# Optimization experiments

Measured on AMD Instinct MI355X. Metric: run time of the kernel, lower is better.

Reference implementation:

```python
import jax, jax.numpy as jnp
import numpy as np

N_NODES = 100000
N_EDGES = 1600000
IN_DIM, HID_DIM, OUT_DIM, N_CLASSES = 128, 256, 256, 200
N_GRAPHS = 64


def gcn_conv(x, edge_index, W, b):
    """PyG GCNConv: add self-loops, symmetric deg^{-1/2} normalization,
    aggregate source->target, then bias. Linear transform applied first
    (cheaper since in/out dims comparable)."""
    N = x.shape[0]
    loop = jnp.arange(N, dtype=edge_index.dtype)
    src = jnp.concatenate([edge_index[0], loop])
    dst = jnp.concatenate([edge_index[1], loop])
    deg = jax.ops.segment_sum(jnp.ones_like(dst, dtype=x.dtype), dst, num_segments=N)
    dinv = jnp.where(deg > 0, jax.lax.rsqrt(deg), 0.0)
    xw = x @ W  # [N, F_out]
    norm = dinv[src] * dinv[dst]  # [E+N]
    msg = xw[src] * norm[:, None]  # gather + scale
    out = jax.ops.segment_sum(msg, dst, num_segments=N)  # scatter-add
    return out + b


def global_mean_pool(x, batch, num_graphs):
    sums = jax.ops.segment_sum(x, batch, num_segments=num_graphs)
    cnt = jax.ops.segment_sum(jnp.ones((x.shape[0],), x.dtype), batch, num_segments=num_graphs)
    return sums / jnp.maximum(cnt, 1.0)[:, None]


def setup_inputs() -> dict:
    key = jax.random.key(0)
    ks = jax.random.split(key, 8)
    x = jax.random.normal(ks[0], (N_NODES, IN_DIM), dtype=jnp.float32)
    edge_index = jax.random.randint(ks[1], (2, N_EDGES), 0, N_NODES, dtype=jnp.int32)
    batch = jnp.sort(jax.random.randint(ks[2], (N_NODES,), 0, N_GRAPHS, dtype=jnp.int32))
    # Glorot-style init for weights (scaled normals)
    W1 = jax.random.normal(ks[3], (IN_DIM, HID_DIM), dtype=jnp.float32) / np.sqrt(IN_DIM)
    b1 = jnp.zeros((HID_DIM,), jnp.float32)
    W2 = jax.random.normal(ks[4], (HID_DIM, OUT_DIM), dtype=jnp.float32) / np.sqrt(HID_DIM)
    b2 = jnp.zeros((OUT_DIM,), jnp.float32)
    Wc = jax.random.normal(ks[5], (OUT_DIM, N_CLASSES), dtype=jnp.float32) / np.sqrt(OUT_DIM)
    bc = jnp.zeros((N_CLASSES,), jnp.float32)
    return {"x": x, "edge_index": edge_index, "batch": batch, "num_graphs": N_GRAPHS,
            "W1": W1, "b1": b1, "W2": W2, "b2": b2, "Wc": Wc, "bc": bc}


def reference(x, edge_index, batch, num_graphs, W1, b1, W2, b2, Wc, bc):
    h = jax.nn.relu(gcn_conv(x, edge_index, W1, b1))
    # dropout p=0.5 is identity in eval mode
    h = jax.nn.relu(gcn_conv(h, edge_index, W2, b2))
    g = global_mean_pool(h, batch, num_graphs)  # [num_graphs, OUT_DIM]
    return g @ Wc + bc  # [num_graphs, N_CLASSES]
```

## Files before the change

kernel.cpp:

```cpp
#include <hip/hip_runtime.h>
#include <cstdint>
#include <cstddef>


typedef __attribute__((ext_vector_type(8))) short bf16x8;
typedef __attribute__((ext_vector_type(4))) float f32x4;

#define P1_CHUNK 4096
#define BCAP 8192

__device__ inline unsigned short f2bf(float f) {
    unsigned u = __float_as_uint(f);
    u = (u + 0x7FFFu + ((u >> 16) & 1u)) >> 16;
    return (unsigned short)u;
}
__device__ inline unsigned nib4(unsigned u) {
    return (u & 15u) | (((u >> 8) & 15u) << 4) | (((u >> 16) & 15u) << 8) |
           (((u >> 24) & 15u) << 12);
}
__device__ inline unsigned nibexp(unsigned h) {
    unsigned t = (h | (h << 8)) & 0x00FF00FFu;
    return (t | (t << 4)) & 0x0F0F0F0Fu;
}
__device__ inline float ub(unsigned u, int q) { return (float)((u >> (8 * q)) & 255u); }

__global__ __launch_bounds__(256) void scatter_prep_kernel(
        const int* __restrict__ src, const int* __restrict__ dst,
        int* __restrict__ bucketCnt, unsigned* __restrict__ pairs, int E, int NB, int EB,
        const float* __restrict__ W1, unsigned short* __restrict__ WT1, int K1,
        const float* __restrict__ W2, unsigned short* __restrict__ WT2,
        const int* __restrict__ batch, int* __restrict__ cnt, int N, int HB,
        const float* __restrict__ x, unsigned char* __restrict__ Y0q,
        float* __restrict__ scaleRaw) {
    __shared__ int hist[512];
    __shared__ int base[512];
    int bid = blockIdx.x, t = threadIdx.x;
    if (bid < EB) {
        int e0 = bid * P1_CHUNK;
        int eend = min(e0 + P1_CHUNK, E);
        for (int i = t; i < NB; i += 256) hist[i] = 0;
        __syncthreads();
        for (int e = e0 + t; e < eend; e += 256) atomicAdd(&hist[dst[e] >> 8], 1);
        __syncthreads();
        for (int i = t; i < NB; i += 256) {
            int c = hist[i];
            base[i] = (c > 0) ? atomicAdd(&bucketCnt[i], c) : 0;
            hist[i] = 0;
        }
        __syncthreads();
        for (int e = e0 + t; e < eend; e += 256) {
            int d = dst[e], s = src[e];
            int b = d >> 8;
            int r = base[b] + atomicAdd(&hist[b], 1);
            if (r < BCAP)
                pairs[(size_t)b * BCAP + r] = (unsigned)s | ((unsigned)(d & 255) << 24);
        }
    } else if (bid < EB + K1) {
        int idx = (bid - EB) * 256 + t;
        int k = idx >> 8, n = idx & 255;
        WT1[n * K1 + k] = f2bf(W1[idx]);
    } else if (bid < EB + K1 + 256) {
        int idx = (bid - EB - K1) * 256 + t;
        int k = idx >> 8, n = idx & 255;
        WT2[n * 256 + k] = f2bf(W2[idx]);
    } else if (bid < EB + K1 + 256 + HB) {
        hist[t] = 0;
        __syncthreads();
        int n = (bid - EB - K1 - 256) * 256 + t;
        if (n < N) atomicAdd(&hist[batch[n]], 1);
        __syncthreads();
        if (hist[t] != 0) atomicAdd(&cnt[t], hist[t]);
    } else {
        int node = (bid - EB - K1 - 256 - HB) * 4 + (t >> 6);
        int lane = t & 63;
        if (node < N) {
            float2 v = reinterpret_cast<const float2*>(x)[(size_t)node * 64 + lane];
            float m = fmaxf(fabsf(v.x), fabsf(v.y));
            #pragma unroll
            for (int d = 32; d >= 1; d >>= 1) m = fmaxf(m, __shfl_xor(m, d, 64));
            float qinv = m > 0.f ? 7.f / m : 0.f;
            int q0 = min(max((int)rintf(v.x * qinv) + 8, 0), 15);
            int q1 = min(max((int)rintf(v.y * qinv) + 8, 0), 15);
            Y0q[(size_t)node * 64 + lane] = (unsigned char)(q0 | (q1 << 4));
            if (lane == 0) scaleRaw[node] = m * (1.f / 7.f);
        }
    }
}

__global__ __launch_bounds__(256) void fine_place_kernel(
        const unsigned* __restrict__ pairs, const int* __restrict__ bucketCnt,
        int* __restrict__ off, float* __restrict__ dinv,
        const float* __restrict__ scaleRaw, float* __restrict__ scale0,
        int* __restrict__ csr, int N, int E) {
    __shared__ int hist[256];
    __shared__ int loff[256];
    __shared__ int ws[4];
    __shared__ int sbase;
    int b = blockIdx.x, t = threadIdx.x;
    int lane = t & 63, w = t >> 6;

    int part = 0;
    for (int i = t; i < b; i += 256) part += bucketCnt[i];
    #pragma unroll
    for (int d = 1; d < 64; d <<= 1) part += __shfl_xor(part, d, 64);
    if (lane == 0) ws[w] = part;
    __syncthreads();
    if (t == 0) sbase = ws[0] + ws[1] + ws[2] + ws[3];
    if (b == 0 && t == 0) off[N] = E;
    __syncthreads();
    int base = sbase;

    int cnt = min(bucketCnt[b], BCAP);
    const unsigned* pp = pairs + (size_t)b * BCAP;
    hist[t] = 0;
    __syncthreads();
    for (int i = t; i < cnt; i += 256) atomicAdd(&hist[pp[i] >> 24], 1);
    __syncthreads();
    int v = hist[t];
    {
        int x = v;
        #pragma unroll
        for (int d = 1; d < 64; d <<= 1) {
            int y = __shfl_up(x, d, 64);
            if (lane >= d) x += y;
        }
        if (lane == 63) ws[w] = x;
        __syncthreads();
        int woff = 0;
        #pragma unroll
        for (int j = 0; j < 4; j++)
            if (j < w) woff += ws[j];
        loff[t] = woff + x - v;
    }
    int node = b * 256 + t;
    if (node < N) {
        off[node] = base + loff[t];
        float di = rsqrtf((float)v + 1.0f);
        dinv[node] = di;
        scale0[node] = di * scaleRaw[node];
    }
    __syncthreads();
    hist[t] = 0;
    __syncthreads();
    for (int i = t; i < cnt; i += 256) {
        unsigned pr = pp[i];
        int dl = pr >> 24;
        int r = atomicAdd(&hist[dl], 1);
        csr[base + loff[dl] + r] = (int)(pr & 0xFFFFFFu);
    }
}

__global__ __launch_bounds__(256) void aggregate_q4x_kernel(
        const unsigned char* __restrict__ Q, const float* __restrict__ scale,
        unsigned short* __restrict__ OUT,
        const int* __restrict__ off, const int* __restrict__ csr,
        const float* __restrict__ dinv, int N) {
    int node = __builtin_amdgcn_readfirstlane(blockIdx.x * 4 + (threadIdx.x >> 6));
    int lane = threadIdx.x & 63;
    if (node >= N) return;

    float acc0, acc1, ssum;
    auto loadpay = [&](int s) -> unsigned {
        return (unsigned)Q[(size_t)s * 64 + lane];
    };
    auto lo = [&](unsigned b) -> float { return (float)(b & 15u); };
    auto hi = [&](unsigned b) -> float { return (float)((b >> 4) & 15u); };
    {
        unsigned v = loadpay(node);
        float sc = scale[node];
        acc0 = sc * lo(v);
        acc1 = sc * hi(v);
        ssum = sc;
    }
    int e0 = off[node], e1 = off[node + 1];
    int e = e0;
    for (; e + 16 <= e1; e += 16) {
        int s[16]; unsigned v[16]; float sc[16];
        #pragma unroll
        for (int j = 0; j < 16; j++) s[j] = csr[e + j];
        #pragma unroll
        for (int j = 0; j < 16; j++) { v[j] = loadpay(s[j]); sc[j] = scale[s[j]]; }
        #pragma unroll
        for (int j = 0; j < 16; j++) {
            ssum += sc[j];
            acc0 += sc[j] * lo(v[j]);
            acc1 += sc[j] * hi(v[j]);
        }
    }
    if (e + 8 <= e1) {
        int s[8]; unsigned v[8]; float sc[8];
        #pragma unroll
        for (int j = 0; j < 8; j++) s[j] = csr[e + j];
        #pragma unroll
        for (int j = 0; j < 8; j++) { v[j] = loadpay(s[j]); sc[j] = scale[s[j]]; }
        #pragma unroll
        for (int j = 0; j < 8; j++) {
            ssum += sc[j];
            acc0 += sc[j] * lo(v[j]);
            acc1 += sc[j] * hi(v[j]);
        }
        e += 8;
    }
    for (; e < e1; e++) {
        int s = csr[e];
        unsigned v = loadpay(s);
        float sc = scale[s];
        ssum += sc;
        acc0 += sc * lo(v);
        acc1 += sc * hi(v);
    }
    float corr = 8.f * ssum;
    float di = dinv[node];
    unsigned o = (unsigned)f2bf(di * (acc0 - corr)) |
                 ((unsigned)f2bf(di * (acc1 - corr)) << 16);
    reinterpret_cast<unsigned*>(OUT)[(size_t)node * 64 + lane] = o;
}

__global__ __launch_bounds__(256) void aggregate_q4_kernel(
        const unsigned short* __restrict__ Q4, const float* __restrict__ scale,
        unsigned short* __restrict__ OUT,
        const int* __restrict__ off, const int* __restrict__ csr,
        const float* __restrict__ dinv, int N) {
    int node = __builtin_amdgcn_readfirstlane(blockIdx.x * 4 + (threadIdx.x >> 6));
    int lane = threadIdx.x & 63;
    if (node >= N) return;

    float acc[4];
    auto loadpay = [&](int s) -> unsigned {
        return (unsigned)Q4[(size_t)s * 64 + lane];
    };
    {
        unsigned u = nibexp(loadpay(node));
        float sc = scale[node];
        #pragma unroll
        for (int q = 0; q < 4; q++) acc[q] = sc * ub(u, q);
    }
    int e0 = off[node], e1 = off[node + 1];
    int e = e0;
    for (; e + 16 <= e1; e += 16) {
        int s[16]; unsigned v[16]; float sc[16];
        #pragma unroll
        for (int j = 0; j < 16; j++) s[j] = csr[e + j];
        #pragma unroll
        for (int j = 0; j < 16; j++) { v[j] = loadpay(s[j]); sc[j] = scale[s[j]]; }
        #pragma unroll
        for (int j = 0; j < 16; j++) {
            unsigned u = nibexp(v[j]);
            #pragma unroll
            for (int q = 0; q < 4; q++) acc[q] += sc[j] * ub(u, q);
        }
    }
    if (e + 8 <= e1) {
        int s[8]; unsigned v[8]; float sc[8];
        #pragma unroll
        for (int j = 0; j < 8; j++) s[j] = csr[e + j];
        #pragma unroll
        for (int j = 0; j < 8; j++) { v[j] = loadpay(s[j]); sc[j] = scale[s[j]]; }
        #pragma unroll
        for (int j = 0; j < 8; j++) {
            unsigned u = nibexp(v[j]);
            #pragma unroll
            for (int q = 0; q < 4; q++) acc[q] += sc[j] * ub(u, q);
        }
        e += 8;
    }
    for (; e < e1; e++) {
        int s = csr[e];
        unsigned u = nibexp(loadpay(s));
        float sc = scale[s];
        #pragma unroll
        for (int q = 0; q < 4; q++) acc[q] += sc * ub(u, q);
    }
    float di = dinv[node];
    uint2 o;
    o.x = (unsigned)f2bf(di * acc[0]) | ((unsigned)f2bf(di * acc[1]) << 16);
    o.y = (unsigned)f2bf(di * acc[2]) | ((unsigned)f2bf(di * acc[3]) << 16);
    reinterpret_cast<uint2*>(OUT)[(size_t)node * 64 + lane] = o;
}

template <int K, int MODE>
__global__ __launch_bounds__(256) void mfma_gemm_kernel(
        const unsigned short* __restrict__ A, const unsigned short* __restrict__ WT,
        const float* __restrict__ bias, const float* __restrict__ dinv,
        char* __restrict__ Cq, float* __restrict__ scaleOut,
        const int* __restrict__ batch, float* __restrict__ gsum, int M) {
    constexpr int KK = K / 32;
    constexpr int RB = K * 2;
    constexpr int CHUNKS = 64 * RB / 16;
    constexpr int EXTRA = (MODE == 0) ? (256 * 4 + 64 * 4 + 64 * 256) : 16;
    __shared__ __align__(16) char As[64 * RB];
    __shared__ __align__(16) char extra[EXTRA];

    const int t = threadIdx.x;
    const int lane = t & 63, w = t >> 6;
    const int lhi = lane >> 4, l15 = lane & 15;
    const int r0 = blockIdx.x * 64;

    bf16x8 breg[4][KK];
    #pragma unroll
    for (int nf = 0; nf < 4; nf++)
        #pragma unroll
        for (int kk = 0; kk < KK; kk++)
            breg[nf][kk] = *reinterpret_cast<const bf16x8*>(
                WT + (size_t)(w * 64 + nf * 16 + l15) * K + kk * 32 + lhi * 8);
    float bn[4];
    #pragma unroll
    for (int nf = 0; nf < 4; nf++) bn[nf] = bias[w * 64 + nf * 16 + l15];

    #pragma unroll
    for (int p = 0; p < CHUNKS / 256; p++) {
        int idx = p * 256 + t;
        int row = idx / (RB / 16);
        int cb = idx % (RB / 16);
        int sbyte = (cb * 16) ^ ((row & 7) << 4);
        const char* g = (const char*)(A + (size_t)(r0 + row) * K) + sbyte;
        __builtin_amdgcn_global_load_lds(
            (const __attribute__((address_space(1))) void*)g,
            (__attribute__((address_space(3))) void*)(As + idx * 16),
            16, 0, 0);
    }
    __syncthreads();

    f32x4 acc[4][4];
    #pragma unroll
    for (int i = 0; i < 4; i++)
        #pragma unroll
        for (int j = 0; j < 4; j++) acc[i][j] = (f32x4){0.f, 0.f, 0.f, 0.f};

    #pragma unroll
    for (int kk = 0; kk < KK; kk++) {
        bf16x8 a[4];
        int kb = (kk * 32 + lhi * 8) * 2;
        #pragma unroll
        for (int mf = 0; mf < 4; mf++) {
            int row = mf * 16 + l15;
            a[mf] = *reinterpret_cast<const bf16x8*>(
                As + row * RB + (kb ^ ((row & 7) << 4)));
        }
        #pragma unroll
        for (int mf = 0; mf < 4; mf++)
            #pragma unroll
            for (int nf = 0; nf < 4; nf++)
                acc[mf][nf] = __builtin_amdgcn_mfma_f32_16x16x32_bf16(
                    a[mf], breg[nf][kk], acc[mf][nf], 0, 0, 0);
    }

    if constexpr (MODE == 0) {
        float* wmax = (float*)extra;
        float* qinv = wmax + 256;
        char* pack = (char*)(qinv + 64);
        #pragma unroll
        for (int mf = 0; mf < 4; mf++)
            #pragma unroll
            for (int j = 0; j < 4; j++) {
                float lmax = 0.f;
                #pragma unroll
                for (int nf = 0; nf < 4; nf++) {
                    float v = fmaxf(acc[mf][nf][j] + bn[nf], 0.f);
                    acc[mf][nf][j] = v;
                    lmax = fmaxf(lmax, v);
                }
                lmax = fmaxf(lmax, __shfl_xor(lmax, 1, 64));
                lmax = fmaxf(lmax, __shfl_xor(lmax, 2, 64));
                lmax = fmaxf(lmax, __shfl_xor(lmax, 4, 64));
                lmax = fmaxf(lmax, __shfl_xor(lmax, 8, 64));
                if (l15 == 0) wmax[w * 64 + mf * 16 + lhi * 4 + j] = lmax;
            }
        __syncthreads();
        if (t < 64) {
            float m4 = fmaxf(fmaxf(wmax[t], wmax[64 + t]),
                             fmaxf(wmax[128 + t], wmax[192 + t]));
            qinv[t] = m4 > 0.f ? 15.f / m4 : 0.f;
            if (r0 + t < M) scaleOut[r0 + t] = dinv[r0 + t] * m4 * (1.f / 15.f);
        }
        __syncthreads();
        #pragma unroll
        for (int mf = 0; mf < 4; mf++)
            #pragma unroll
            for (int j = 0; j < 4; j++) {
                int r = mf * 16 + lhi * 4 + j;
                float qi = qinv[r];
                #pragma unroll
                for (int nf = 0; nf < 4; nf++)
                    pack[r * 256 + w * 64 + nf * 16 + l15] =
                        (char)min((int)rintf(acc[mf][nf][j] * qi), 15);
            }
        __syncthreads();
        #pragma unroll
        for (int p = 0; p < 4; p++) {
            int idx = p * 256 + t;
            uint4 s4 = reinterpret_cast<const uint4*>(pack)[idx];
            uint2 o;
            o.x = nib4(s4.x) | (nib4(s4.y) << 16);
            o.y = nib4(s4.z) | (nib4(s4.w) << 16);
            reinterpret_cast<uint2*>(Cq + (size_t)r0 * 128)[idx] = o;
        }
    } else {
        int gmin = batch[min(r0, M - 1)];
        int gmax = batch[min(r0 + 63, M - 1)];
        if (gmin == gmax) {
            #pragma unroll
            for (int nf = 0; nf < 4; nf++) {
                float s = 0.f;
                #pragma unroll
                for (int mf = 0; mf < 4; mf++)
                    #pragma unroll
                    for (int j = 0; j < 4; j++) {
                        int m = r0 + mf * 16 + lhi * 4 + j;
                        float v = fmaxf(acc[mf][nf][j] + bn[nf], 0.f);
                        s += (m < M) ? v : 0.f;
                    }
                s += __shfl_xor(s, 16, 64);
                s += __shfl_xor(s, 32, 64);
                if (lhi == 0)
                    atomicAdd(&gsum[(size_t)gmin * 256 + w * 64 + nf * 16 + l15], s);
            }
        } else {
            #pragma unroll
            for (int mf = 0; mf < 4; mf++)
                #pragma unroll
                for (int j = 0; j < 4; j++) {
                    int m = r0 + mf * 16 + lhi * 4 + j;
                    if (m < M) {
                        int g = batch[m];
                        #pragma unroll
                        for (int nf = 0; nf < 4; nf++)
                            atomicAdd(&gsum[(size_t)g * 256 + w * 64 + nf * 16 + l15],
                                      fmaxf(acc[mf][nf][j] + bn[nf], 0.f));
                    }
                }
        }
    }
}

__global__ __launch_bounds__(256) void pool_final_kernel(const float* __restrict__ gsum,
                                                         const int* __restrict__ cnt,
                                                         const float* __restrict__ Wc,
                                                         const float* __restrict__ bc,
                                                         float* __restrict__ out) {
    __shared__ float gm[256];
    int g = blockIdx.x, t = threadIdx.x;
    float inv = 1.0f / fmaxf((float)cnt[g], 1.0f);
    gm[t] = gsum[g * 256 + t] * inv;
    __syncthreads();
    if (t < 200) {
        float acc = bc[t];
        #pragma unroll 8
        for (int k = 0; k < 256; k++) acc += gm[k] * Wc[k * 200 + t];
        out[g * 200 + t] = acc;
    }
}

extern "C" void kernel_launch(void* const* d_in, const int* in_sizes, int n_in,
                              void* d_out, int out_size, void* d_ws, size_t ws_size,
                              hipStream_t stream) {
    const float* x   = (const float*)d_in[0];
    const int* ei    = (const int*)d_in[1];
    const int* batch = (const int*)d_in[2];
    const float* W1  = (const float*)d_in[4];
    const float* b1  = (const float*)d_in[5];
    const float* W2  = (const float*)d_in[6];
    const float* b2  = (const float*)d_in[7];
    const float* Wc  = (const float*)d_in[8];
    const float* bc  = (const float*)d_in[9];
    float* out = (float*)d_out;

    const int N = in_sizes[2];
    const int E = in_sizes[1] / 2;
    const int G = out_size / 200;
    const int K1 = in_sizes[0] / N;
    const int Mpad = (N + 63) & ~63;
    const int NB = (N + 255) >> 8;
    const int ntiles = Mpad / 64;
    const int EB = (E + P1_CHUNK - 1) / P1_CHUNK;
    const int* src = ei;
    const int* dst = ei + E;

    char* p = (char*)d_ws;
    auto alloc = [&](size_t bytes) -> char* {
        char* r = p;
        p += (bytes + 255) & ~(size_t)255;
        return r;
    };
    int*   off      = (int*)alloc((size_t)(N + 1) * 4);
    int*   bktCnt   = (int*)alloc((size_t)NB * 4);
    int*   cnt      = (int*)alloc(256 * 4);
    float* dinv     = (float*)alloc((size_t)N * 4);
    float* scaleRaw = (float*)alloc((size_t)N * 4);
    float* scale0   = (float*)alloc((size_t)N * 4);
    float* scale1   = (float*)alloc((size_t)N * 4);
    float* gsum     = (float*)alloc((size_t)G * 256 * 4);
    int*   csr      = (int*)alloc((size_t)E * 4);
    unsigned* pairs = (unsigned*)alloc((size_t)NB * BCAP * 4);
    unsigned short* WT1 = (unsigned short*)alloc((size_t)256 * K1 * 2);
    unsigned short* WT2 = (unsigned short*)alloc((size_t)256 * 256 * 2);
    unsigned char*  Y0q4 = (unsigned char*)alloc((size_t)N * 64);
    char*           Y1q4 = alloc((size_t)Mpad * 128);
    unsigned short* a1   = (unsigned short*)alloc((size_t)Mpad * K1 * 2);
    unsigned short* a2   = (unsigned short*)alloc((size_t)Mpad * 256 * 2);

    hipMemsetAsync(bktCnt, 0, (size_t)NB * 4, stream);
    hipMemsetAsync(cnt, 0, 256 * 4, stream);
    hipMemsetAsync(gsum, 0, (size_t)G * 256 * 4, stream);

    int blkN = (N + 255) / 256;
    int PB = (N + 3) / 4;
    scatter_prep_kernel<<<EB + K1 + 256 + blkN + PB, 256, 0, stream>>>(
        src, dst, bktCnt, pairs, E, NB, EB, W1, WT1, K1, W2, WT2,
        batch, cnt, N, blkN, x, Y0q4, scaleRaw);
    fine_place_kernel<<<NB, 256, 0, stream>>>(
        pairs, bktCnt, off, dinv, scaleRaw, scale0, csr, N, E);

    aggregate_q4x_kernel<<<(N + 3) / 4, 256, 0, stream>>>(
        Y0q4, scale0, a1, off, csr, dinv, N);
    mfma_gemm_kernel<128, 0><<<ntiles, 256, 0, stream>>>(
        a1, WT1, b1, dinv, Y1q4, scale1, nullptr, nullptr, N);
    aggregate_q4_kernel<<<(N + 3) / 4, 256, 0, stream>>>(
        (const unsigned short*)Y1q4, scale1, a2, off, csr, dinv, N);
    mfma_gemm_kernel<256, 1><<<ntiles, 256, 0, stream>>>(
        a2, WT2, b2, nullptr, nullptr, nullptr, batch, gsum, N);
    pool_final_kernel<<<G, 256, 0, stream>>>(gsum, cnt, Wc, bc, out);
}
```

Baseline: 269.9 us.

## Overlap GEMM tiles with aggregation chunks via fused role-split kernels

Splits each layer's node range into three chunks and launches fused kernels in which one block in seventeen runs a GEMM tile for the previous chunk while the remaining blocks aggregate the next chunk. The goal is to hide the compute-bound MFMA GEMM behind the memory-bound gather. Fused GEMM blocks load weights from global memory per MFMA instead of holding them in registers, which keeps the fused kernel's register use within the occupancy hint but re-reads weights inside the inner loop. The change also adds more launches and a large shared-memory footprint to the aggregation blocks, which may lower their occupancy.

```diff
diff --git a/kernel.cpp b/kernel.cpp
--- a/kernel.cpp
+++ b/kernel.cpp
@@ -150,27 +150,20 @@
     }
 }
 
-__global__ __launch_bounds__(256) void aggregate_q4x_kernel(
+
+__device__ __forceinline__ void agg_q4x_body(
         const unsigned char* __restrict__ Q, const float* __restrict__ scale,
         unsigned short* __restrict__ OUT,
         const int* __restrict__ off, const int* __restrict__ csr,
-        const float* __restrict__ dinv, int N) {
-    int node = __builtin_amdgcn_readfirstlane(blockIdx.x * 4 + (threadIdx.x >> 6));
-    int lane = threadIdx.x & 63;
-    if (node >= N) return;
-
+        const float* __restrict__ dinv, int node, int lane) {
     float acc0, acc1, ssum;
-    auto loadpay = [&](int s) -> unsigned {
-        return (unsigned)Q[(size_t)s * 64 + lane];
-    };
+    auto loadpay = [&](int s) -> unsigned { return (unsigned)Q[(size_t)s * 64 + lane]; };
     auto lo = [&](unsigned b) -> float { return (float)(b & 15u); };
     auto hi = [&](unsigned b) -> float { return (float)((b >> 4) & 15u); };
     {
         unsigned v = loadpay(node);
         float sc = scale[node];
-        acc0 = sc * lo(v);
-        acc1 = sc * hi(v);
-        ssum = sc;
+        acc0 = sc * lo(v); acc1 = sc * hi(v); ssum = sc;
     }
     int e0 = off[node], e1 = off[node + 1];
     int e = e0;
@@ -181,11 +174,7 @@
         #pragma unroll
         for (int j = 0; j < 16; j++) { v[j] = loadpay(s[j]); sc[j] = scale[s[j]]; }
         #pragma unroll
-        for (int j = 0; j < 16; j++) {
-            ssum += sc[j];
-            acc0 += sc[j] * lo(v[j]);
-            acc1 += sc[j] * hi(v[j]);
-        }
+        for (int j = 0; j < 16; j++) { ssum += sc[j]; acc0 += sc[j] * lo(v[j]); acc1 += sc[j] * hi(v[j]); }
     }
     if (e + 8 <= e1) {
         int s[8]; unsigned v[8]; float sc[8];
@@ -194,20 +183,14 @@
         #pragma unroll
         for (int j = 0; j < 8; j++) { v[j] = loadpay(s[j]); sc[j] = scale[s[j]]; }
         #pragma unroll
-        for (int j = 0; j < 8; j++) {
-            ssum += sc[j];
-            acc0 += sc[j] * lo(v[j]);
-            acc1 += sc[j] * hi(v[j]);
-        }
+        for (int j = 0; j < 8; j++) { ssum += sc[j]; acc0 += sc[j] * lo(v[j]); acc1 += sc[j] * hi(v[j]); }
         e += 8;
     }
     for (; e < e1; e++) {
         int s = csr[e];
         unsigned v = loadpay(s);
         float sc = scale[s];
-        ssum += sc;
-        acc0 += sc * lo(v);
-        acc1 += sc * hi(v);
+        ssum += sc; acc0 += sc * lo(v); acc1 += sc * hi(v);
     }
     float corr = 8.f * ssum;
     float di = dinv[node];
@@ -216,19 +199,13 @@
     reinterpret_cast<unsigned*>(OUT)[(size_t)node * 64 + lane] = o;
 }
 
-__global__ __launch_bounds__(256) void aggregate_q4_kernel(
+__device__ __forceinline__ void agg_q4_body(
         const unsigned short* __restrict__ Q4, const float* __restrict__ scale,
         unsigned short* __restrict__ OUT,
         const int* __restrict__ off, const int* __restrict__ csr,
-        const float* __restrict__ dinv, int N) {
-    int node = __builtin_amdgcn_readfirstlane(blockIdx.x * 4 + (threadIdx.x >> 6));
-    int lane = threadIdx.x & 63;
-    if (node >= N) return;
-
+        const float* __restrict__ dinv, int node, int lane) {
     float acc[4];
-    auto loadpay = [&](int s) -> unsigned {
-        return (unsigned)Q4[(size_t)s * 64 + lane];
-    };
+    auto loadpay = [&](int s) -> unsigned { return (unsigned)Q4[(size_t)s * 64 + lane]; };
     {
         unsigned u = nibexp(loadpay(node));
         float sc = scale[node];
@@ -278,31 +255,31 @@
     reinterpret_cast<uint2*>(OUT)[(size_t)node * 64 + lane] = o;
 }
 
-template <int K, int MODE>
-__global__ __launch_bounds__(256) void mfma_gemm_kernel(
+template <int K, int MODE, bool BREG>
+__device__ __forceinline__ void gemm_body(
         const unsigned short* __restrict__ A, const unsigned short* __restrict__ WT,
         const float* __restrict__ bias, const float* __restrict__ dinv,
         char* __restrict__ Cq, float* __restrict__ scaleOut,
-        const int* __restrict__ batch, float* __restrict__ gsum, int M) {
+        const int* __restrict__ batch, float* __restrict__ gsum,
+        int M, int r0, char* As, char* extra) {
     constexpr int KK = K / 32;
     constexpr int RB = K * 2;
     constexpr int CHUNKS = 64 * RB / 16;
-    constexpr int EXTRA = (MODE == 0) ? (256 * 4 + 64 * 4 + 64 * 256) : 16;
-    __shared__ __align__(16) char As[64 * RB];
-    __shared__ __align__(16) char extra[EXTRA];
-
     const int t = threadIdx.x;
     const int lane = t & 63, w = t >> 6;
     const int lhi = lane >> 4, l15 = lane & 15;
-    const int r0 = blockIdx.x * 64;
-
+
+    auto bload = [&](int nf, int kk) -> bf16x8 {
+        return *reinterpret_cast<const bf16x8*>(
+            WT + (size_t)(w * 64 + nf * 16 + l15) * K + kk * 32 + lhi * 8);
+    };
     bf16x8 breg[4][KK];
-    #pragma unroll
-    for (int nf = 0; nf < 4; nf++)
-        #pragma unroll
-        for (int kk = 0; kk < KK; kk++)
-            breg[nf][kk] = *reinterpret_cast<const bf16x8*>(
-                WT + (size_t)(w * 64 + nf * 16 + l15) * K + kk * 32 + lhi * 8);
+    if constexpr (BREG) {
+        #pragma unroll
+        for (int nf = 0; nf < 4; nf++)
+            #pragma unroll
+            for (int kk = 0; kk < KK; kk++) breg[nf][kk] = bload(nf, kk);
+    }
     float bn[4];
     #pragma unroll
     for (int nf = 0; nf < 4; nf++) bn[nf] = bias[w * 64 + nf * 16 + l15];
@@ -340,9 +317,13 @@
         #pragma unroll
         for (int mf = 0; mf < 4; mf++)
             #pragma unroll
-            for (int nf = 0; nf < 4; nf++)
+            for (int nf = 0; nf < 4; nf++) {
+                bf16x8 bv;
+                if constexpr (BREG) bv = breg[nf][kk];
+                else bv = bload(nf, kk);
                 acc[mf][nf] = __builtin_amdgcn_mfma_f32_16x16x32_bf16(
-                    a[mf], breg[nf][kk], acc[mf][nf], 0, 0, 0);
+                    a[mf], bv, acc[mf][nf], 0, 0, 0);
+            }
     }
 
     if constexpr (MODE == 0) {
@@ -430,6 +411,87 @@
                     }
                 }
         }
+    }
+}
+
+
+__global__ __launch_bounds__(256) void aggregate_q4x_kernel(
+        const unsigned char* __restrict__ Q, const float* __restrict__ scale,
+        unsigned short* __restrict__ OUT,
+        const int* __restrict__ off, const int* __restrict__ csr,
+        const float* __restrict__ dinv, int nodeStart, int nodeEnd) {
+    int node = __builtin_amdgcn_readfirstlane(nodeStart + blockIdx.x * 4 + (threadIdx.x >> 6));
+    if (node < nodeEnd)
+        agg_q4x_body(Q, scale, OUT, off, csr, dinv, node, threadIdx.x & 63);
+}
+
+__global__ __launch_bounds__(256) void aggregate_q4_kernel(
+        const unsigned short* __restrict__ Q4, const float* __restrict__ scale,
+        unsigned short* __restrict__ OUT,
+        const int* __restrict__ off, const int* __restrict__ csr,
+        const float* __restrict__ dinv, int nodeStart, int nodeEnd) {
+    int node = __builtin_amdgcn_readfirstlane(nodeStart + blockIdx.x * 4 + (threadIdx.x >> 6));
+    if (node < nodeEnd)
+        agg_q4_body(Q4, scale, OUT, off, csr, dinv, node, threadIdx.x & 63);
+}
+
+template <int K, int MODE>
+__global__ __launch_bounds__(256) void mfma_gemm_kernel(
+        const unsigned short* __restrict__ A, const unsigned short* __restrict__ WT,
+        const float* __restrict__ bias, const float* __restrict__ dinv,
+        char* __restrict__ Cq, float* __restrict__ scaleOut,
+        const int* __restrict__ batch, float* __restrict__ gsum, int M, int rowStart) {
+    __shared__ __align__(16) char As[64 * K * 2];
+    __shared__ __align__(16) char extra[(MODE == 0) ? (256 * 4 + 64 * 4 + 64 * 256) : 16];
+    gemm_body<K, MODE, true>(A, WT, bias, dinv, Cq, scaleOut, batch, gsum,
+                             M, rowStart + blockIdx.x * 64, As, extra);
+}
+
+__device__ __forceinline__ bool role_split(int bid, int G, int& gemmIdx, int& aggIdx) {
+    if (bid % 17 == 0 && bid / 17 < G) { gemmIdx = bid / 17; return true; }
+    aggIdx = bid - min((bid + 16) / 17, G);
+    return false;
+}
+
+__global__ __launch_bounds__(256, 4) void fused_l1_kernel(
+        const unsigned char* __restrict__ Q0, const float* __restrict__ scale0,
+        unsigned short* __restrict__ a1,
+        const int* __restrict__ off, const int* __restrict__ csr,
+        const float* __restrict__ dinv,
+        const unsigned short* __restrict__ WT1, const float* __restrict__ b1,
+        char* __restrict__ Y1q4, float* __restrict__ scale1,
+        int N, int gemmTiles, int aggStart, int aggEnd, int gemmStart) {
+    __shared__ __align__(16) char As[64 * 256];
+    __shared__ __align__(16) char extra[256 * 4 + 64 * 4 + 64 * 256];
+    int gi, ai;
+    if (role_split(blockIdx.x, gemmTiles, gi, ai)) {
+        gemm_body<128, 0, false>(a1, WT1, b1, dinv, Y1q4, scale1, nullptr, nullptr,
+                                 N, gemmStart + gi * 64, As, extra);
+    } else {
+        int node = __builtin_amdgcn_readfirstlane(aggStart + ai * 4 + (threadIdx.x >> 6));
+        if (node < aggEnd)
+            agg_q4x_body(Q0, scale0, a1, off, csr, dinv, node, threadIdx.x & 63);
+    }
+}
+
+__global__ __launch_bounds__(256, 4) void fused_l2_kernel(
+        const unsigned short* __restrict__ Y1q4, const float* __restrict__ scale1,
+        unsigned short* __restrict__ a2,
+        const int* __restrict__ off, const int* __restrict__ csr,
+        const float* __restrict__ dinv,
+        const unsigned short* __restrict__ WT2, const float* __restrict__ b2,
+        const int* __restrict__ batch, float* __restrict__ gsum,
+        int N, int gemmTiles, int aggStart, int aggEnd, int gemmStart) {
+    __shared__ __align__(16) char As[64 * 512];
+    __shared__ __align__(16) char extra[16];
+    int gi, ai;
+    if (role_split(blockIdx.x, gemmTiles, gi, ai)) {
+        gemm_body<256, 1, false>(a2, WT2, b2, nullptr, nullptr, nullptr, batch, gsum,
+                                 N, gemmStart + gi * 64, As, extra);
+    } else {
+        int node = __builtin_amdgcn_readfirstlane(aggStart + ai * 4 + (threadIdx.x >> 6));
+        if (node < aggEnd)
+            agg_q4_body(Y1q4, scale1, a2, off, csr, dinv, node, threadIdx.x & 63);
     }
 }
 
@@ -511,13 +573,34 @@
     fine_place_kernel<<<NB, 256, 0, stream>>>(
         pairs, bktCnt, off, dinv, scaleRaw, scale0, csr, N, E);
 
-    aggregate_q4x_kernel<<<(N + 3) / 4, 256, 0, stream>>>(
-        Y0q4, scale0, a1, off, csr, dinv, N);
-    mfma_gemm_kernel<128, 0><<<ntiles, 256, 0, stream>>>(
-        a1, WT1, b1, dinv, Y1q4, scale1, nullptr, nullptr, N);
-    aggregate_q4_kernel<<<(N + 3) / 4, 256, 0, stream>>>(
-        (const unsigned short*)Y1q4, scale1, a2, off, csr, dinv, N);
-    mfma_gemm_kernel<256, 1><<<ntiles, 256, 0, stream>>>(
-        a2, WT2, b2, nullptr, nullptr, nullptr, batch, gsum, N);
+    const int CT = ntiles / 3;
+    const int RC = CT * 64;
+    const int T2 = ntiles - 2 * CT;
+    int end0 = min(RC, N), end1 = min(2 * RC, N);
+    int ab0 = (end0 + 3) / 4;
+    int ab1 = (end1 - RC + 3) / 4;
+    int ab2 = (N - 2 * RC + 3) / 4;
+
+    aggregate_q4x_kernel<<<ab0, 256, 0, stream>>>(Y0q4, scale0, a1, off, csr, dinv, 0, end0);
+    fused_l1_kernel<<<ab1 + CT, 256, 0, stream>>>(
+        Y0q4, scale0, a1, off, csr, dinv, WT1, b1, Y1q4, scale1,
+        N, CT, RC, end1, 0);
+    fused_l1_kernel<<<ab2 + CT, 256, 0, stream>>>(
+        Y0q4, scale0, a1, off, csr, dinv, WT1, b1, Y1q4, scale1,
+        N, CT, 2 * RC, N, RC);
+    mfma_gemm_kernel<128, 0><<<T2, 256, 0, stream>>>(
+        a1, WT1, b1, dinv, Y1q4, scale1, nullptr, nullptr, N, 2 * RC);
+
+    aggregate_q4_kernel<<<ab0, 256, 0, stream>>>(
+        (const unsigned short*)Y1q4, scale1, a2, off, csr, dinv, 0, end0);
+    fused_l2_kernel<<<ab1 + CT, 256, 0, stream>>>(
+        (const unsigned short*)Y1q4, scale1, a2, off, csr, dinv, WT2, b2,
+        batch, gsum, N, CT, RC, end1, 0);
+    fused_l2_kernel<<<ab2 + CT, 256, 0, stream>>>(
+        (const unsigned short*)Y1q4, scale1, a2, off, csr, dinv, WT2, b2,
+        batch, gsum, N, CT, 2 * RC, N, RC);
+    mfma_gemm_kernel<256, 1><<<T2, 256, 0, stream>>>(
+        a2, WT2, b2, nullptr, nullptr, nullptr, batch, gsum, N, 2 * RC);
+
     pool_final_kernel<<<G, 256, 0, stream>>>(gsum, cnt, Wc, bc, out);
 }
```

Measured after the change: 359.6 us. 33.2% more time.
